# Kernel optimization log

Measured on AMD Instinct MI355X. Metric: run time of the kernel, lower is better.

## Reference

```python
import jax, jax.numpy as jnp
import numpy as np

NEG_SLOPE = 0.2  # PyG GATConv leaky_relu slope


def gat_conv(x, src, dst, W, a_src, a_dst, bias, heads, out_ch, concat, n_nodes):
    # x: [N, in], W: [heads*out_ch, in], a_src/a_dst: [heads, out_ch]
    h = (x @ W.T).reshape(n_nodes, heads, out_ch)          # [N,H,C]
    alpha_src = (h * a_src).sum(-1)                         # [N,H]
    alpha_dst = (h * a_dst).sum(-1)                         # [N,H]
    e = jax.nn.leaky_relu(alpha_src[src] + alpha_dst[dst], NEG_SLOPE)  # [E,H]
    # segment softmax over incoming edges of each dst node (self-loops ensure non-empty)
    m = jax.ops.segment_max(e, dst, num_segments=n_nodes)
    e = jnp.exp(e - m[dst])
    s = jax.ops.segment_sum(e, dst, num_segments=n_nodes)
    alpha = e / (s[dst] + 1e-16)                            # [E,H]
    msg = h[src] * alpha[:, :, None]                        # [E,H,C]
    out = jax.ops.segment_sum(msg, dst, num_segments=n_nodes)  # [N,H,C]
    out = out.reshape(n_nodes, heads * out_ch) if concat else out.mean(axis=1)
    return out + bias


def setup_inputs() -> dict:
    key = jax.random.key(0)
    ks = jax.random.split(key, 16)
    N, E, IN, HID, OUT, H1, H2 = 10000, 160000, 256, 32, 32, 8, 10
    inp = {
        "x": jax.random.normal(ks[0], (N, IN), dtype=jnp.float32),
        "edge_index": jax.random.randint(ks[1], (2, E), 0, N, dtype=jnp.int64),
        # GATConv 1: in=256 -> 8 heads x 32
        "W1": jax.random.normal(ks[2], (H1 * HID, IN), dtype=jnp.float32) * 0.05,
        "a1s": jax.random.normal(ks[3], (H1, HID), dtype=jnp.float32) * 0.05,
        "a1d": jax.random.normal(ks[4], (H1, HID), dtype=jnp.float32) * 0.05,
        "b1": jnp.zeros((H1 * HID,), dtype=jnp.float32),
        # GATConv 2: in=256 -> 8 heads x 32
        "W2": jax.random.normal(ks[5], (H1 * HID, H1 * HID), dtype=jnp.float32) * 0.05,
        "a2s": jax.random.normal(ks[6], (H1, HID), dtype=jnp.float32) * 0.05,
        "a2d": jax.random.normal(ks[7], (H1, HID), dtype=jnp.float32) * 0.05,
        "b2": jnp.zeros((H1 * HID,), dtype=jnp.float32),
        # GATConv 3: in=256 -> 10 heads x 32, concat=False (mean)
        "W3": jax.random.normal(ks[8], (H2 * OUT, H1 * HID), dtype=jnp.float32) * 0.05,
        "a3s": jax.random.normal(ks[9], (H2, OUT), dtype=jnp.float32) * 0.05,
        "a3d": jax.random.normal(ks[10], (H2, OUT), dtype=jnp.float32) * 0.05,
        "b3": jnp.zeros((OUT,), dtype=jnp.float32),
        # residual projections
        "P1W": jax.random.normal(ks[11], (H1 * HID, IN), dtype=jnp.float32) * 0.05,
        "P1b": jnp.zeros((H1 * HID,), dtype=jnp.float32),
        "P3W": jax.random.normal(ks[12], (OUT, H1 * HID), dtype=jnp.float32) * 0.05,
        "P3b": jnp.zeros((OUT,), dtype=jnp.float32),
    }
    return inp


def reference(x, edge_index, W1, a1s, a1d, b1, W2, a2s, a2d, b2,
              W3, a3s, a3d, b3, P1W, P1b, P3W, P3b):
    N = x.shape[0]
    loop = jnp.arange(N, dtype=edge_index.dtype)
    src = jnp.concatenate([edge_index[0], loop])  # PyG adds self-loops by default
    dst = jnp.concatenate([edge_index[1], loop])

    identity1 = x @ P1W.T + P1b
    h = gat_conv(x, src, dst, W1, a1s, a1d, b1, 8, 32, True, N)
    h = jax.nn.elu(h) + identity1  # dropout inactive in eval

    identity2 = h
    h2 = gat_conv(h, src, dst, W2, a2s, a2d, b2, 8, 32, True, N)
    h = jax.nn.elu(h2) + identity2

    identity3 = h @ P3W.T + P3b
    h3 = gat_conv(h, src, dst, W3, a3s, a3d, b3, 10, 32, False, N)
    return h3 + identity3
```

## Files before the change

### kernel.cpp

```cpp
#include <hip/hip_runtime.h>
#include <hip/hip_bf16.h>

typedef __hip_bfloat16 bf16;
typedef __attribute__((ext_vector_type(8))) short bf16x8;
typedef __attribute__((ext_vector_type(4))) short bf16x4;
typedef __attribute__((ext_vector_type(4))) float f32x4;


static __device__ __forceinline__ float bf2f(bf16 v) { return __bfloat162float(v); }
static __device__ __forceinline__ float bf2fs(short v) {
    unsigned int u = ((unsigned int)(unsigned short)v) << 16;
    return __builtin_bit_cast(float, u);
}
static __device__ __forceinline__ short f2bfs(float f) {
    bf16 b = __float2bfloat16(f);
    return __builtin_bit_cast(short, b);
}
static __device__ __forceinline__ float loadf(const void* p, size_t i, int isf32) {
    return isf32 ? ((const float*)p)[i] : bf2f(((const bf16*)p)[i]);
}
static __device__ __forceinline__ int get_isf32(const int* flags) {
    return (flags[0] | (flags[2] == 0)) ? 1 : 0;
}

__global__ void k_zero(int* __restrict__ flags, int* __restrict__ cnt, int N) {
    int i = blockIdx.x * blockDim.x + threadIdx.x;
    if (i < 4) flags[i] = 0;
    for (; i < N; i += gridDim.x * blockDim.x) cnt[i] = 0;
}

__global__ void k_detect(const unsigned short* __restrict__ xu, const int* __restrict__ ew,
                         int* __restrict__ flags, int nx, int ne2, int bx) {
    __shared__ int lf[3];
    if (threadIdx.x < 3) lf[threadIdx.x] = 0;
    __syncthreads();
    if ((int)blockIdx.x < bx) {
        for (int i = blockIdx.x * 256 + threadIdx.x; i < nx; i += bx * 256) {
            unsigned short v = xu[i];
            if ((v & 0x7F80u) == 0x7F80u) lf[0] = 1;
            if (((i & 1) == 0) && v != 0) lf[2] = 1;
        }
    } else {
        int nb = gridDim.x - bx;
        for (int i = (blockIdx.x - bx) * 256 + threadIdx.x; i < ne2; i += nb * 256) {
            if ((i & 1) && ew[i] != 0) lf[1] = 1;
        }
    }
    __syncthreads();
    if (threadIdx.x == 0) {
        if (lf[0]) atomicOr(&flags[0], 1);
        if (lf[1]) atomicOr(&flags[1], 1);
        if (lf[2]) atomicOr(&flags[2], 1);
    }
}

static __device__ __forceinline__ void cast8(const void* src, bf16* dst, int i8, int isf32) {
    if (isf32) {
        f32x4 a = ((const f32x4*)src)[2 * i8];
        f32x4 b = ((const f32x4*)src)[2 * i8 + 1];
        bf16x8 o;
        o[0] = f2bfs(a[0]); o[1] = f2bfs(a[1]); o[2] = f2bfs(a[2]); o[3] = f2bfs(a[3]);
        o[4] = f2bfs(b[0]); o[5] = f2bfs(b[1]); o[6] = f2bfs(b[2]); o[7] = f2bfs(b[3]);
        ((bf16x8*)dst)[i8] = o;
    } else {
        ((bf16x8*)dst)[i8] = ((const bf16x8*)src)[i8];
    }
}

__global__ void k_cast_all(const void* s0, bf16* d0, int c0,
                           const void* s1, bf16* d1, int c1,
                           const void* s2, bf16* d2, int c2,
                           const void* s3, bf16* d3, int c3,
                           const void* s4, bf16* d4, int c4,
                           const void* s5, bf16* d5, int c5,
                           const int* __restrict__ flags) {
    int t = blockIdx.x * blockDim.x + threadIdx.x;
    int isf32 = get_isf32(flags);
    if (t < c0) { cast8(s0, d0, t, isf32); return; } t -= c0;
    if (t < c1) { cast8(s1, d1, t, isf32); return; } t -= c1;
    if (t < c2) { cast8(s2, d2, t, isf32); return; } t -= c2;
    if (t < c3) { cast8(s3, d3, t, isf32); return; } t -= c3;
    if (t < c4) { cast8(s4, d4, t, isf32); return; } t -= c4;
    if (t < c5) { cast8(s5, d5, t, isf32); }
}

__global__ void k_norm_count(const int* __restrict__ w, const int* __restrict__ flags,
                             int* __restrict__ s, int* __restrict__ d,
                             int* __restrict__ cnt, int E) {
    int e = blockIdx.x * blockDim.x + threadIdx.x;
    if (e >= E) return;
    int sv, dv;
    if (flags[1] == 0) {
        sv = w[2 * (size_t)e];
        dv = w[2 * (size_t)E + 2 * (size_t)e];
    } else {
        sv = w[e];
        dv = w[(size_t)E + e];
    }
    s[e] = sv;
    d[e] = dv;
    atomicAdd(&cnt[dv], 1);
}

__global__ void k_scan(int* __restrict__ cnt, int* __restrict__ row_ptr, int N) {
    __shared__ int part[1024];
    int tid = threadIdx.x;
    int vpt = (N + 1023) >> 10;
    int i0 = tid * vpt;
    int i1 = i0 + vpt; if (i1 > N) i1 = N;
    int s = 0;
    for (int i = i0; i < i1; ++i) s += cnt[i] + 1;
    part[tid] = s;
    __syncthreads();
    for (int off = 1; off < 1024; off <<= 1) {
        int t = (tid >= off) ? part[tid - off] : 0;
        __syncthreads();
        part[tid] += t;
        __syncthreads();
    }
    int run = (tid == 0) ? 0 : part[tid - 1];
    for (int i = i0; i < i1; ++i) {
        int c = cnt[i] + 1;
        cnt[i] = run;
        run += c;
        row_ptr[i + 1] = run;
    }
    if (tid == 0) row_ptr[0] = 0;
}

__global__ void k_fill(const int* __restrict__ edst, int* __restrict__ cursor,
                       const int* __restrict__ row_ptr, int* __restrict__ csr_e,
                       int E, int N) {
    int e = blockIdx.x * blockDim.x + threadIdx.x;
    if (e < E) {
        int d = edst[e];
        int pos = atomicAdd(&cursor[d], 1);
        csr_e[pos] = e;
    } else if (e < E + N) {
        int d = e - E;
        csr_e[row_ptr[d + 1] - 1] = e;
    }
}

template<int NT>
__global__ void k_gemm_split(const bf16* __restrict__ A, const bf16* __restrict__ W,
                             const void* __restrict__ bias1, const int* __restrict__ flags,
                             bf16* __restrict__ out0, int S0, int ld0,
                             bf16* __restrict__ out1, int ld1, int n1,
                             int M, int Fo, int K,
                             const void* __restrict__ aS, const void* __restrict__ aD,
                             float* __restrict__ asrc, float* __restrict__ adst, int H) {
    int wid = threadIdx.x >> 6;
    int lane = threadIdx.x & 63;
    int mrow = blockIdx.x * 64 + wid * 16;
    if (mrow >= M) return;
    int ncol = blockIdx.y * (NT * 16);
    int r = lane & 15, g = lane >> 4;

    f32x4 acc[NT];
#pragma unroll
    for (int t = 0; t < NT; ++t) acc[t] = (f32x4){0.f, 0.f, 0.f, 0.f};

    const bf16* arow = A + (size_t)(mrow + r) * K + g * 8;
    const bf16* wbase = W + (size_t)(ncol + r) * K + g * 8;
    for (int k0 = 0; k0 < K; k0 += 32) {
        bf16x8 af = *(const bf16x8*)(arow + k0);
#pragma unroll
        for (int t = 0; t < NT; ++t) {
            bf16x8 bfr = *(const bf16x8*)(wbase + (size_t)t * 16 * K + k0);
            acc[t] = __builtin_amdgcn_mfma_f32_16x16x32_bf16(af, bfr, acc[t], 0, 0, 0);
        }
    }
    int isf32 = get_isf32(flags);

#pragma unroll
    for (int t = 0; t < NT; ++t) {
        int n = ncol + t * 16 + r;
        bool is0 = n < S0;
        int jc = n - S0;
        float bv = (!is0 && jc < n1 && bias1) ? loadf(bias1, jc, isf32) : 0.f;
#pragma unroll
        for (int j = 0; j < 4; ++j) {
            int m = mrow + 4 * g + j;
            float v = acc[t][j] + bv;
            if (is0) out0[(size_t)m * ld0 + n] = __float2bfloat16(v);
            else if (jc < n1) out1[(size_t)m * ld1 + jc] = __float2bfloat16(v);
        }
    }

    if (aS && ncol < S0) {
        float ps[2][4], pd[2][4];
#pragma unroll
        for (int hb = 0; hb < 2; ++hb)
#pragma unroll
            for (int j = 0; j < 4; ++j) { ps[hb][j] = 0.f; pd[hb][j] = 0.f; }
#pragma unroll
        for (int t = 0; t < NT; ++t) {
            int col = ncol + t * 16 + r;
            float asv = loadf(aS, col, isf32);
            float adv = loadf(aD, col, isf32);
#pragma unroll
            for (int j = 0; j < 4; ++j) {
                ps[t >> 1][j] += acc[t][j] * asv;
                pd[t >> 1][j] += acc[t][j] * adv;
            }
        }
#pragma unroll
        for (int mk = 1; mk <= 8; mk <<= 1) {
#pragma unroll
            for (int hb = 0; hb < 2; ++hb)
#pragma unroll
                for (int j = 0; j < 4; ++j) {
                    ps[hb][j] += __shfl_xor(ps[hb][j], mk);
                    pd[hb][j] += __shfl_xor(pd[hb][j], mk);
                }
        }
        if (r == 0) {
            int hA = ncol >> 5, hB = hA + 1;
#pragma unroll
            for (int j = 0; j < 4; ++j) {
                int m = mrow + 4 * g + j;
                asrc[(size_t)m * H + hA] = ps[0][j];
                asrc[(size_t)m * H + hB] = ps[1][j];
                adst[(size_t)m * H + hA] = pd[0][j];
                adst[(size_t)m * H + hB] = pd[1][j];
            }
        }
    }
}

#define CAP 96
__global__ void k_fused_agg(const bf16* __restrict__ hlin,
                            const float* __restrict__ asrc, const float* __restrict__ adst,
                            const int* __restrict__ esrc, const int* __restrict__ row_ptr,
                            const int* __restrict__ csr_e,
                            const void* __restrict__ bias, const bf16* __restrict__ identb,
                            void* __restrict__ out, bf16* __restrict__ outb,
                            const int* __restrict__ flags,
                            int E, int N, int H, int mode) {
    __shared__ float el[4][CAP * 10];
    __shared__ int   ssrc[4][CAP];
    __shared__ float idn[4][10];
    int wid = threadIdx.x >> 6, lane = threadIdx.x & 63;
    int d = blockIdx.x * 4 + wid;
    bool active = d < N;
    int isf32 = get_isf32(flags);
    int F = H * 32;
    int nj = (F + 255) >> 8;
    int lo = 0, deg = 0;
    if (active) { lo = row_ptr[d]; deg = row_ptr[d + 1] - lo; }
    bool fast = deg <= CAP;

    if (active && fast) {
        int EC = 64 / H;
        int h = lane % H, ei = lane / H;
        float ad = adst[(size_t)d * H + h];
        for (int base = 0; base < deg; base += EC) {
            int p = base + ei;
            if (ei < EC && p < deg) {
                int e = csr_e[lo + p];
                int s = (e < E) ? esrc[e] : (e - E);
                float v = asrc[(size_t)s * H + h] + ad;
                v = (v > 0.f) ? v : 0.2f * v;
                el[wid][p * H + h] = v;
                if (h == 0) ssrc[wid][p] = s;
            }
        }
    }
    __syncthreads();
    if (active && fast) {
        if (H == 8) {
            int h = lane & 7, sub = lane >> 3;
            float m = -1e30f;
            for (int p = sub; p < deg; p += 8) m = fmaxf(m, el[wid][p * 8 + h]);
            m = fmaxf(m, __shfl_xor(m, 8));
            m = fmaxf(m, __shfl_xor(m, 16));
            m = fmaxf(m, __shfl_xor(m, 32));
            float den = 0.f;
            for (int p = sub; p < deg; p += 8) {
                float t = __expf(el[wid][p * 8 + h] - m);
                el[wid][p * 8 + h] = t;
                den += t;
            }
            den += __shfl_xor(den, 8);
            den += __shfl_xor(den, 16);
            den += __shfl_xor(den, 32);
            if (lane < 8) idn[wid][lane] = 1.f / (den + 1e-16f);
        } else if (lane < H) {
            float m = -1e30f;
            for (int p = 0; p < deg; ++p) m = fmaxf(m, el[wid][p * H + lane]);
            float den = 0.f;
            for (int p = 0; p < deg; ++p) {
                float t = __expf(el[wid][p * H + lane] - m);
                el[wid][p * H + lane] = t;
                den += t;
            }
            idn[wid][lane] = 1.f / (den + 1e-16f);
        }
    }
    __syncthreads();
    if (!active) return;

    if (mode == 1 && fast) {
        int g = lane & 15, q = lane >> 4;
        int f0 = g * 16;
        f32x4 a0 = {0.f,0.f,0.f,0.f}, a1 = {0.f,0.f,0.f,0.f};
        f32x4 a2 = {0.f,0.f,0.f,0.f}, a3 = {0.f,0.f,0.f,0.f};
        for (int p = q; p < deg; p += 4) {
            int s = ssrc[wid][p];
            const bf16* hp = hlin + (size_t)s * 256 + f0;
            bf16x8 h0 = *(const bf16x8*)hp;
            bf16x8 h1 = *(const bf16x8*)(hp + 8);
            float w = el[wid][p * 8 + (g >> 1)];
#pragma unroll
            for (int k = 0; k < 4; ++k) {
                a0[k] += w * bf2fs(h0[k]);
                a1[k] += w * bf2fs(h0[4 + k]);
                a2[k] += w * bf2fs(h1[k]);
                a3[k] += w * bf2fs(h1[4 + k]);
            }
        }
#pragma unroll
        for (int k = 0; k < 4; ++k) {
            a0[k] += __shfl_xor(a0[k], 16); a1[k] += __shfl_xor(a1[k], 16);
            a2[k] += __shfl_xor(a2[k], 16); a3[k] += __shfl_xor(a3[k], 16);
            a0[k] += __shfl_xor(a0[k], 32); a1[k] += __shfl_xor(a1[k], 32);
            a2[k] += __shfl_xor(a2[k], 32); a3[k] += __shfl_xor(a3[k], 32);
        }
        if (lane < 16) {
            float inv = idn[wid][g >> 1];
            const bf16* idp = identb + (size_t)d * 256 + f0;
            bf16x8 id0 = *(const bf16x8*)idp;
            bf16x8 id1 = *(const bf16x8*)(idp + 8);
            bf16* ob = outb + (size_t)d * 256 + f0;
            f32x4 av[4] = {a0, a1, a2, a3};
            bf16x8 obv0, obv1;
#pragma unroll
            for (int i = 0; i < 4; ++i) {
#pragma unroll
                for (int k = 0; k < 4; ++k) {
                    float v = av[i][k] * inv + loadf(bias, f0 + 4 * i + k, isf32);
                    v = (v > 0.f) ? v : (__expf(v) - 1.f);
                    int e8 = 4 * i + k;
                    v += bf2fs((e8 < 8) ? id0[e8] : id1[e8 - 8]);
                    if (i < 2) obv0[e8] = f2bfs(v);
                    else       obv1[e8 - 8] = f2bfs(v);
                }
            }
            *(bf16x8*)ob = obv0;
            *(bf16x8*)(ob + 8) = obv1;
        }
        return;
    }

    if (mode == 2 && fast) {
        int g = lane & 15, q = lane >> 4;
        int f0 = g * 16;
        int f1 = 256 + g * 4;
        f32x4 a0 = {0.f,0.f,0.f,0.f}, a1 = {0.f,0.f,0.f,0.f};
        f32x4 a2 = {0.f,0.f,0.f,0.f}, a3 = {0.f,0.f,0.f,0.f};
        f32x4 a4 = {0.f,0.f,0.f,0.f};
        for (int p = q; p < deg; p += 4) {
            int s = ssrc[wid][p];
            const bf16* hp = hlin + (size_t)s * 320;
            bf16x8 h0 = *(const bf16x8*)(hp + f0);
            bf16x8 h1 = *(const bf16x8*)(hp + f0 + 8);
            bf16x4 h2 = *(const bf16x4*)(hp + f1);
            float w0 = el[wid][p * 10 + (g >> 1)];
            float w2 = el[wid][p * 10 + 8 + (g >> 3)];
#pragma unroll
            for (int k = 0; k < 4; ++k) {
                a0[k] += w0 * bf2fs(h0[k]);
                a1[k] += w0 * bf2fs(h0[4 + k]);
                a2[k] += w0 * bf2fs(h1[k]);
                a3[k] += w0 * bf2fs(h1[4 + k]);
                a4[k] += w2 * bf2fs(h2[k]);
            }
        }
#pragma unroll
        for (int k = 0; k < 4; ++k) {
            a0[k] += __shfl_xor(a0[k], 16); a1[k] += __shfl_xor(a1[k], 16);
            a2[k] += __shfl_xor(a2[k], 16); a3[k] += __shfl_xor(a3[k], 16);
            a4[k] += __shfl_xor(a4[k], 16);
            a0[k] += __shfl_xor(a0[k], 32); a1[k] += __shfl_xor(a1[k], 32);
            a2[k] += __shfl_xor(a2[k], 32); a3[k] += __shfl_xor(a3[k], 32);
            a4[k] += __shfl_xor(a4[k], 32);
        }
        float* scratch = &el[wid][0];
        if (lane < 16) {
            float inv0 = idn[wid][g >> 1];
            float inv2 = idn[wid][8 + (g >> 3)];
#pragma unroll
            for (int k = 0; k < 4; ++k) {
                scratch[f0 + k]      = a0[k] * inv0;
                scratch[f0 + 4 + k]  = a1[k] * inv0;
                scratch[f0 + 8 + k]  = a2[k] * inv0;
                scratch[f0 + 12 + k] = a3[k] * inv0;
                scratch[f1 + k]      = a4[k] * inv2;
            }
        }
        if (lane < 32) {
            float s = 0.f;
#pragma unroll
            for (int h = 0; h < 10; ++h) s += scratch[h * 32 + lane];
            float v = s * 0.1f + loadf(bias, lane, isf32)
                    + bf2f(identb[(size_t)d * 32 + lane]);
            if (isf32) ((float*)out)[(size_t)d * 32 + lane] = v;
            else ((bf16*)out)[(size_t)d * 32 + lane] = __float2bfloat16(v);
        }
        return;
    }

    f32x4 acc[2] = {(f32x4){0.f,0.f,0.f,0.f}, (f32x4){0.f,0.f,0.f,0.f}};
    for (int j = 0; j < nj; ++j) {
        int f0 = (lane + 64 * j) * 4;
        if (f0 >= F) continue;
        int hj = f0 >> 5;
        float ad = adst[(size_t)d * H + hj];
        float m = -1e30f;
        for (int p = 0; p < deg; ++p) {
            int e = csr_e[lo + p];
            int s = (e < E) ? esrc[e] : (e - E);
            float v = asrc[(size_t)s * H + hj] + ad;
            v = (v > 0.f) ? v : 0.2f * v;
            m = fmaxf(m, v);
        }
        float den = 0.f;
        f32x4 a4 = {0.f, 0.f, 0.f, 0.f};
        for (int p = 0; p < deg; ++p) {
            int e = csr_e[lo + p];
            int s = (e < E) ? esrc[e] : (e - E);
            float v = asrc[(size_t)s * H + hj] + ad;
            v = (v > 0.f) ? v : 0.2f * v;
            float t = __expf(v - m);
            den += t;
            bf16x4 hv = *(const bf16x4*)(hlin + (size_t)s * F + f0);
            for (int k = 0; k < 4; ++k) a4[k] += t * bf2fs(hv[k]);
        }
        float inv = 1.f / (den + 1e-16f);
        for (int k = 0; k < 4; ++k) acc[j][k] = a4[k] * inv;
    }
    if (mode == 1) {
        int f0 = lane * 4;
        bf16x4 ob;
#pragma unroll
        for (int k = 0; k < 4; ++k) {
            float v = acc[0][k] + loadf(bias, f0 + k, isf32);
            v = (v > 0.f) ? v : (__expf(v) - 1.f);
            v += bf2f(identb[(size_t)d * F + f0 + k]);
            ob[k] = f2bfs(v);
        }
        *(bf16x4*)(outb + (size_t)d * F + f0) = ob;
    } else {
        float* scratch = &el[wid][0];
#pragma unroll
        for (int j = 0; j < 2; ++j) {
            int f0 = (lane + 64 * j) * 4;
            if (j < nj && f0 < F) {
#pragma unroll
                for (int k = 0; k < 4; ++k) scratch[f0 + k] = acc[j][k];
            }
        }
        if (lane < 32) {
            float s = 0.f;
            for (int h = 0; h < H; ++h) s += scratch[h * 32 + lane];
            float v = s * (1.f / (float)H) + loadf(bias, lane, isf32)
                    + bf2f(identb[(size_t)d * 32 + lane]);
            if (isf32) ((float*)out)[(size_t)d * 32 + lane] = v;
            else ((bf16*)out)[(size_t)d * 32 + lane] = __float2bfloat16(v);
        }
    }
}

extern "C" void kernel_launch(void* const* d_in, const int* in_sizes, int n_in,
                              void* d_out, int out_size, void* d_ws, size_t ws_size,
                              hipStream_t stream) {
    const int IN = 256, C = 32;
    const int N = in_sizes[0] / IN;
    const int E = in_sizes[1] / 2;
    const int ET = E + N;

    const void* x    = d_in[0];
    const int*  edge = (const int*)d_in[1];
    const void* W1 = d_in[2];
    const void* a1s = d_in[3];
    const void* a1d = d_in[4];
    const void* b1 = d_in[5];
    const void* W2 = d_in[6];
    const void* a2s = d_in[7];
    const void* a2d = d_in[8];
    const void* b2 = d_in[9];
    const void* W3 = d_in[10];
    const void* a3s = d_in[11];
    const void* a3d = d_in[12];
    const void* b3 = d_in[13];
    const void* P1W = d_in[14];
    const void* P1b = d_in[15];
    const void* P3W = d_in[16];
    const void* P3b = d_in[17];

    char* ws = (char*)d_ws;
    size_t off = 0;
    auto alloc = [&](size_t bytes) -> void* {
        void* p = ws + off;
        off = (off + bytes + 255) & ~(size_t)255;
        return p;
    };
    bf16* fxb   = (bf16*)alloc((size_t)N * 256 * 2);
    bf16* fyb   = (bf16*)alloc((size_t)N * 256 * 2);
    bf16* fhb   = (bf16*)alloc((size_t)N * 320 * 2);
    bf16* fidb  = (bf16*)alloc((size_t)N * 256 * 2);
    float* fasrc = (float*)alloc((size_t)N * 10 * 4);
    float* fadst = (float*)alloc((size_t)N * 10 * 4);
    bf16* wc1   = (bf16*)alloc((size_t)512 * 256 * 2);
    bf16* wb2   = (bf16*)alloc((size_t)256 * 256 * 2);
    bf16* wc3   = (bf16*)alloc((size_t)384 * 256 * 2);
    int*  isrc  = (int*)alloc((size_t)E * 4);
    int*  idst  = (int*)alloc((size_t)E * 4);
    int*  irow  = (int*)alloc((size_t)(N + 1) * 4);
    int*  icur  = (int*)alloc((size_t)N * 4);
    int*  icsr  = (int*)alloc((size_t)ET * 4);
    int*  flags = (int*)alloc(4 * 4);
    (void)ws_size;

    auto cdiv = [](int a, int b) { return (a + b - 1) / b; };

    k_zero<<<cdiv(N, 256), 256, 0, stream>>>(flags, icur, N);

    int nprobe_x = (N * 256 < 16384) ? N * 256 : 16384;
    int nprobe_e = (2 * E < 8192) ? 2 * E : 8192;
    int bx = cdiv(nprobe_x, 256) < 16 ? cdiv(nprobe_x, 256) : 16;
    int be = cdiv(nprobe_e, 256) < 8 ? cdiv(nprobe_e, 256) : 8;
    k_detect<<<bx + be, 256, 0, stream>>>(
        (const unsigned short*)x, edge, flags, nprobe_x, nprobe_e, bx);

    int c_x = N * 256 / 8, c_w = 256 * 256 / 8, c_w3 = 320 * 256 / 8, c_p3 = 32 * 256 / 8;
    int ctot = c_x + 3 * c_w + c_w3 + c_p3;
    k_cast_all<<<cdiv(ctot, 256), 256, 0, stream>>>(
        x, fxb, c_x,
        W1, wc1, c_w,
        P1W, wc1 + (size_t)256 * 256, c_w,
        W2, wb2, c_w,
        W3, wc3, c_w3,
        P3W, wc3 + (size_t)320 * 256, c_p3,
        flags);

    k_norm_count<<<cdiv(E, 256), 256, 0, stream>>>(edge, flags, isrc, idst, icur, E);
    k_scan<<<1, 1024, 0, stream>>>(icur, irow, N);
    k_fill<<<cdiv(ET, 256), 256, 0, stream>>>(idst, icur, irow, icsr, E, N);

    int gx = cdiv(N, 64);
    int ga = cdiv(N, 4);

    {
        int H = 8;
        k_gemm_split<4><<<dim3(gx, 8), 256, 0, stream>>>(
            fxb, wc1, P1b, flags, fhb, 256, 256, fidb, 256, 256, N, 512, 256,
            a1s, a1d, fasrc, fadst, H);
        k_fused_agg<<<ga, 256, 0, stream>>>(fhb, fasrc, fadst, isrc, irow, icsr,
                                            b1, fidb, nullptr, fyb, flags, E, N, H, 1);
    }
    {
        int H = 8;
        k_gemm_split<4><<<dim3(gx, 4), 256, 0, stream>>>(
            fyb, wb2, nullptr, flags, fhb, 256, 256, nullptr, 0, 0, N, 256, 256,
            a2s, a2d, fasrc, fadst, H);
        k_fused_agg<<<ga, 256, 0, stream>>>(fhb, fasrc, fadst, isrc, irow, icsr,
                                            b2, fyb, nullptr, fyb, flags, E, N, H, 1);
    }
    {
        int H = 10;
        k_gemm_split<4><<<dim3(gx, 6), 256, 0, stream>>>(
            fyb, wc3, P3b, flags, fhb, 320, 320, fidb, 32, 32, N, 384, 256,
            a3s, a3d, fasrc, fadst, H);
        k_fused_agg<<<ga, 256, 0, stream>>>(fhb, fasrc, fadst, isrc, irow, icsr,
                                            b3, fidb, d_out, nullptr, flags, E, N, H, 2);
    }
}
```

Before: 202.9 us.

## Merge setup kernels and unroll gather loops over two edges

Folds the zeroing and format-detection kernels into one launch, where a single block probes the input format and writes the flags directly and the other blocks zero the counts. The cast kernel and the edge normalisation/count kernel are also merged into one grid. Together this removes two kernel launches and their serialisation gaps. The aggregation loops for modes 1 and 2 now handle two source rows per iteration, so more gather loads are in flight at once, at the cost of more registers and a remainder path.

```diff
diff --git a/kernel.cpp b/kernel.cpp
--- a/kernel.cpp
+++ b/kernel.cpp
@@ -23,34 +23,32 @@
     return (flags[0] | (flags[2] == 0)) ? 1 : 0;
 }
 
-__global__ void k_zero(int* __restrict__ flags, int* __restrict__ cnt, int N) {
-    int i = blockIdx.x * blockDim.x + threadIdx.x;
-    if (i < 4) flags[i] = 0;
-    for (; i < N; i += gridDim.x * blockDim.x) cnt[i] = 0;
-}
-
-__global__ void k_detect(const unsigned short* __restrict__ xu, const int* __restrict__ ew,
-                         int* __restrict__ flags, int nx, int ne2, int bx) {
-    __shared__ int lf[3];
-    if (threadIdx.x < 3) lf[threadIdx.x] = 0;
-    __syncthreads();
-    if ((int)blockIdx.x < bx) {
-        for (int i = blockIdx.x * 256 + threadIdx.x; i < nx; i += bx * 256) {
+__global__ void k_init(const unsigned short* __restrict__ xu, const int* __restrict__ ew,
+                       int* __restrict__ flags, int* __restrict__ cnt,
+                       int N, int nx, int ne2) {
+    if (blockIdx.x == 0) {
+        __shared__ int lf[3];
+        if (threadIdx.x < 3) lf[threadIdx.x] = 0;
+        __syncthreads();
+        int f0 = 0, f1 = 0, f2 = 0;
+        for (int i = threadIdx.x; i < nx; i += 256) {
             unsigned short v = xu[i];
-            if ((v & 0x7F80u) == 0x7F80u) lf[0] = 1;
-            if (((i & 1) == 0) && v != 0) lf[2] = 1;
+            if ((v & 0x7F80u) == 0x7F80u) f0 = 1;
+            if (((i & 1) == 0) && v != 0) f2 = 1;
+        }
+        for (int i = threadIdx.x; i < ne2; i += 256) {
+            if ((i & 1) && ew[i] != 0) f1 = 1;
+        }
+        if (f0) lf[0] = 1;
+        if (f1) lf[1] = 1;
+        if (f2) lf[2] = 1;
+        __syncthreads();
+        if (threadIdx.x == 0) {
+            flags[0] = lf[0]; flags[1] = lf[1]; flags[2] = lf[2]; flags[3] = 0;
         }
     } else {
-        int nb = gridDim.x - bx;
-        for (int i = (blockIdx.x - bx) * 256 + threadIdx.x; i < ne2; i += nb * 256) {
-            if ((i & 1) && ew[i] != 0) lf[1] = 1;
-        }
-    }
-    __syncthreads();
-    if (threadIdx.x == 0) {
-        if (lf[0]) atomicOr(&flags[0], 1);
-        if (lf[1]) atomicOr(&flags[1], 1);
-        if (lf[2]) atomicOr(&flags[2], 1);
+        for (int i = (blockIdx.x - 1) * 256 + threadIdx.x; i < N;
+             i += (gridDim.x - 1) * 256) cnt[i] = 0;
     }
 }
 
@@ -67,39 +65,39 @@
     }
 }
 
-__global__ void k_cast_all(const void* s0, bf16* d0, int c0,
-                           const void* s1, bf16* d1, int c1,
-                           const void* s2, bf16* d2, int c2,
-                           const void* s3, bf16* d3, int c3,
-                           const void* s4, bf16* d4, int c4,
-                           const void* s5, bf16* d5, int c5,
-                           const int* __restrict__ flags) {
-    int t = blockIdx.x * blockDim.x + threadIdx.x;
-    int isf32 = get_isf32(flags);
-    if (t < c0) { cast8(s0, d0, t, isf32); return; } t -= c0;
-    if (t < c1) { cast8(s1, d1, t, isf32); return; } t -= c1;
-    if (t < c2) { cast8(s2, d2, t, isf32); return; } t -= c2;
-    if (t < c3) { cast8(s3, d3, t, isf32); return; } t -= c3;
-    if (t < c4) { cast8(s4, d4, t, isf32); return; } t -= c4;
-    if (t < c5) { cast8(s5, d5, t, isf32); }
-}
-
-__global__ void k_norm_count(const int* __restrict__ w, const int* __restrict__ flags,
-                             int* __restrict__ s, int* __restrict__ d,
-                             int* __restrict__ cnt, int E) {
-    int e = blockIdx.x * blockDim.x + threadIdx.x;
-    if (e >= E) return;
-    int sv, dv;
-    if (flags[1] == 0) {
-        sv = w[2 * (size_t)e];
-        dv = w[2 * (size_t)E + 2 * (size_t)e];
+__global__ void k_cast_norm(const void* s0, bf16* d0, int c0,
+                            const void* s1, bf16* d1, int c1,
+                            const void* s2, bf16* d2, int c2,
+                            const void* s3, bf16* d3, int c3,
+                            const void* s4, bf16* d4, int c4,
+                            const void* s5, bf16* d5, int c5,
+                            const int* __restrict__ w, int* __restrict__ es,
+                            int* __restrict__ ed, int* __restrict__ cnt, int E,
+                            const int* __restrict__ flags, int cb) {
+    if ((int)blockIdx.x < cb) {
+        int t = blockIdx.x * 256 + threadIdx.x;
+        int isf32 = get_isf32(flags);
+        if (t < c0) { cast8(s0, d0, t, isf32); return; } t -= c0;
+        if (t < c1) { cast8(s1, d1, t, isf32); return; } t -= c1;
+        if (t < c2) { cast8(s2, d2, t, isf32); return; } t -= c2;
+        if (t < c3) { cast8(s3, d3, t, isf32); return; } t -= c3;
+        if (t < c4) { cast8(s4, d4, t, isf32); return; } t -= c4;
+        if (t < c5) { cast8(s5, d5, t, isf32); }
     } else {
-        sv = w[e];
-        dv = w[(size_t)E + e];
-    }
-    s[e] = sv;
-    d[e] = dv;
-    atomicAdd(&cnt[dv], 1);
+        int e = (blockIdx.x - cb) * 256 + threadIdx.x;
+        if (e >= E) return;
+        int sv, dv;
+        if (flags[1] == 0) {
+            sv = w[2 * (size_t)e];
+            dv = w[2 * (size_t)E + 2 * (size_t)e];
+        } else {
+            sv = w[e];
+            dv = w[(size_t)E + e];
+        }
+        es[e] = sv;
+        ed[e] = dv;
+        atomicAdd(&cnt[dv], 1);
+    }
 }
 
 __global__ void k_scan(int* __restrict__ cnt, int* __restrict__ row_ptr, int N) {
@@ -306,18 +304,42 @@
         int f0 = g * 16;
         f32x4 a0 = {0.f,0.f,0.f,0.f}, a1 = {0.f,0.f,0.f,0.f};
         f32x4 a2 = {0.f,0.f,0.f,0.f}, a3 = {0.f,0.f,0.f,0.f};
-        for (int p = q; p < deg; p += 4) {
-            int s = ssrc[wid][p];
-            const bf16* hp = hlin + (size_t)s * 256 + f0;
-            bf16x8 h0 = *(const bf16x8*)hp;
-            bf16x8 h1 = *(const bf16x8*)(hp + 8);
-            float w = el[wid][p * 8 + (g >> 1)];
+        int p = q;
+        for (; p + 4 < deg; p += 8) {
+            int s0 = ssrc[wid][p];
+            int s1 = ssrc[wid][p + 4];
+            const bf16* hp0 = hlin + (size_t)s0 * 256 + f0;
+            const bf16* hp1 = hlin + (size_t)s1 * 256 + f0;
+            bf16x8 u0 = *(const bf16x8*)hp0;
+            bf16x8 u1 = *(const bf16x8*)(hp0 + 8);
+            bf16x8 v0 = *(const bf16x8*)hp1;
+            bf16x8 v1 = *(const bf16x8*)(hp1 + 8);
+            float w0 = el[wid][p * 8 + (g >> 1)];
+            float w1 = el[wid][(p + 4) * 8 + (g >> 1)];
 #pragma unroll
             for (int k = 0; k < 4; ++k) {
-                a0[k] += w * bf2fs(h0[k]);
-                a1[k] += w * bf2fs(h0[4 + k]);
-                a2[k] += w * bf2fs(h1[k]);
-                a3[k] += w * bf2fs(h1[4 + k]);
+                a0[k] += w0 * bf2fs(u0[k]);
+                a1[k] += w0 * bf2fs(u0[4 + k]);
+                a2[k] += w0 * bf2fs(u1[k]);
+                a3[k] += w0 * bf2fs(u1[4 + k]);
+                a0[k] += w1 * bf2fs(v0[k]);
+                a1[k] += w1 * bf2fs(v0[4 + k]);
+                a2[k] += w1 * bf2fs(v1[k]);
+                a3[k] += w1 * bf2fs(v1[4 + k]);
+            }
+        }
+        if (p < deg) {
+            int s0 = ssrc[wid][p];
+            const bf16* hp0 = hlin + (size_t)s0 * 256 + f0;
+            bf16x8 u0 = *(const bf16x8*)hp0;
+            bf16x8 u1 = *(const bf16x8*)(hp0 + 8);
+            float w0 = el[wid][p * 8 + (g >> 1)];
+#pragma unroll
+            for (int k = 0; k < 4; ++k) {
+                a0[k] += w0 * bf2fs(u0[k]);
+                a1[k] += w0 * bf2fs(u0[4 + k]);
+                a2[k] += w0 * bf2fs(u1[k]);
+                a3[k] += w0 * bf2fs(u1[4 + k]);
             }
         }
 #pragma unroll
@@ -360,21 +382,51 @@
         f32x4 a0 = {0.f,0.f,0.f,0.f}, a1 = {0.f,0.f,0.f,0.f};
         f32x4 a2 = {0.f,0.f,0.f,0.f}, a3 = {0.f,0.f,0.f,0.f};
         f32x4 a4 = {0.f,0.f,0.f,0.f};
-        for (int p = q; p < deg; p += 4) {
-            int s = ssrc[wid][p];
-            const bf16* hp = hlin + (size_t)s * 320;
-            bf16x8 h0 = *(const bf16x8*)(hp + f0);
-            bf16x8 h1 = *(const bf16x8*)(hp + f0 + 8);
-            bf16x4 h2 = *(const bf16x4*)(hp + f1);
-            float w0 = el[wid][p * 10 + (g >> 1)];
-            float w2 = el[wid][p * 10 + 8 + (g >> 3)];
+        int p = q;
+        for (; p + 4 < deg; p += 8) {
+            int s0 = ssrc[wid][p];
+            int s1 = ssrc[wid][p + 4];
+            const bf16* hp0 = hlin + (size_t)s0 * 320;
+            const bf16* hp1 = hlin + (size_t)s1 * 320;
+            bf16x8 u0 = *(const bf16x8*)(hp0 + f0);
+            bf16x8 u1 = *(const bf16x8*)(hp0 + f0 + 8);
+            bf16x4 u2 = *(const bf16x4*)(hp0 + f1);
+            bf16x8 v0 = *(const bf16x8*)(hp1 + f0);
+            bf16x8 v1 = *(const bf16x8*)(hp1 + f0 + 8);
+            bf16x4 v2 = *(const bf16x4*)(hp1 + f1);
+            float w00 = el[wid][p * 10 + (g >> 1)];
+            float w02 = el[wid][p * 10 + 8 + (g >> 3)];
+            float w10 = el[wid][(p + 4) * 10 + (g >> 1)];
+            float w12 = el[wid][(p + 4) * 10 + 8 + (g >> 3)];
 #pragma unroll
             for (int k = 0; k < 4; ++k) {
-                a0[k] += w0 * bf2fs(h0[k]);
-                a1[k] += w0 * bf2fs(h0[4 + k]);
-                a2[k] += w0 * bf2fs(h1[k]);
-                a3[k] += w0 * bf2fs(h1[4 + k]);
-                a4[k] += w2 * bf2fs(h2[k]);
+                a0[k] += w00 * bf2fs(u0[k]);
+                a1[k] += w00 * bf2fs(u0[4 + k]);
+                a2[k] += w00 * bf2fs(u1[k]);
+                a3[k] += w00 * bf2fs(u1[4 + k]);
+                a4[k] += w02 * bf2fs(u2[k]);
+                a0[k] += w10 * bf2fs(v0[k]);
+                a1[k] += w10 * bf2fs(v0[4 + k]);
+                a2[k] += w10 * bf2fs(v1[k]);
+                a3[k] += w10 * bf2fs(v1[4 + k]);
+                a4[k] += w12 * bf2fs(v2[k]);
+            }
+        }
+        if (p < deg) {
+            int s0 = ssrc[wid][p];
+            const bf16* hp0 = hlin + (size_t)s0 * 320;
+            bf16x8 u0 = *(const bf16x8*)(hp0 + f0);
+            bf16x8 u1 = *(const bf16x8*)(hp0 + f0 + 8);
+            bf16x4 u2 = *(const bf16x4*)(hp0 + f1);
+            float w00 = el[wid][p * 10 + (g >> 1)];
+            float w02 = el[wid][p * 10 + 8 + (g >> 3)];
+#pragma unroll
+            for (int k = 0; k < 4; ++k) {
+                a0[k] += w00 * bf2fs(u0[k]);
+                a1[k] += w00 * bf2fs(u0[4 + k]);
+                a2[k] += w00 * bf2fs(u1[k]);
+                a3[k] += w00 * bf2fs(u1[4 + k]);
+                a4[k] += w02 * bf2fs(u2[k]);
             }
         }
 #pragma unroll
@@ -525,27 +577,23 @@
 
     auto cdiv = [](int a, int b) { return (a + b - 1) / b; };
 
-    k_zero<<<cdiv(N, 256), 256, 0, stream>>>(flags, icur, N);
-
     int nprobe_x = (N * 256 < 16384) ? N * 256 : 16384;
     int nprobe_e = (2 * E < 8192) ? 2 * E : 8192;
-    int bx = cdiv(nprobe_x, 256) < 16 ? cdiv(nprobe_x, 256) : 16;
-    int be = cdiv(nprobe_e, 256) < 8 ? cdiv(nprobe_e, 256) : 8;
-    k_detect<<<bx + be, 256, 0, stream>>>(
-        (const unsigned short*)x, edge, flags, nprobe_x, nprobe_e, bx);
+    k_init<<<1 + cdiv(N, 256), 256, 0, stream>>>(
+        (const unsigned short*)x, edge, flags, icur, N, nprobe_x, nprobe_e);
 
     int c_x = N * 256 / 8, c_w = 256 * 256 / 8, c_w3 = 320 * 256 / 8, c_p3 = 32 * 256 / 8;
     int ctot = c_x + 3 * c_w + c_w3 + c_p3;
-    k_cast_all<<<cdiv(ctot, 256), 256, 0, stream>>>(
+    int cb = cdiv(ctot, 256);
+    k_cast_norm<<<cb + cdiv(E, 256), 256, 0, stream>>>(
         x, fxb, c_x,
         W1, wc1, c_w,
         P1W, wc1 + (size_t)256 * 256, c_w,
         W2, wb2, c_w,
         W3, wc3, c_w3,
         P3W, wc3 + (size_t)320 * 256, c_p3,
-        flags);
-
-    k_norm_count<<<cdiv(E, 256), 256, 0, stream>>>(edge, flags, isrc, idst, icur, E);
+        edge, isrc, idst, icur, E, flags, cb);
+
     k_scan<<<1, 1024, 0, stream>>>(icur, irow, N);
     k_fill<<<cdiv(ET, 256), 256, 0, stream>>>(idst, icur, irow, icsr, E, N);
 
```

After: 220.7 us. +8.8%, slower.
